# Performance work log

Measured on AMD Instinct MI355X. Metric: run time of the kernel, lower is better.

The kernel has to match this reference:

```python
import jax, jax.numpy as jnp
import numpy as np

FORGET_BIAS = 1.0  # tf.nn.rnn_cell.LSTMCell default

def lstm_scan(x_seq, W, b, reverse=False):
    # x_seq: [B, T, D]; W: [D+U, 4U] with TF gate order (i, j, f, o); b: [4U]
    B = x_seq.shape[0]
    U = b.shape[0] // 4
    xs = jnp.swapaxes(x_seq, 0, 1)  # [T, B, D]

    def step(carry, x_t):
        c, h = carry
        z = jnp.dot(jnp.concatenate([x_t, h], axis=-1), W) + b  # [B, 4U]
        i, j, f, o = jnp.split(z, 4, axis=-1)
        c_new = jax.nn.sigmoid(f + FORGET_BIAS) * c + jax.nn.sigmoid(i) * jnp.tanh(j)
        h_new = jax.nn.sigmoid(o) * jnp.tanh(c_new)
        return (c_new, h_new), h_new

    init = (jnp.zeros((B, U), x_seq.dtype), jnp.zeros((B, U), x_seq.dtype))
    _, hs = jax.lax.scan(step, init, xs, reverse=reverse)  # outputs aligned to time index
    return jnp.swapaxes(hs, 0, 1)  # [B, T, U]

def setup_inputs() -> dict:
    key = jax.random.key(0)
    k1, k2, k3 = jax.random.split(key, 3)
    B, H, W_, C = 64, 8, 512, 64
    D, U = H * C, 256
    scale = 1.0 / np.sqrt(D + U)
    x = jax.random.normal(k1, (B, H, W_, C), dtype=jnp.float32)
    W_fw = jax.random.normal(k2, (D + U, 4 * U), dtype=jnp.float32) * scale
    W_bw = jax.random.normal(k3, (D + U, 4 * U), dtype=jnp.float32) * scale
    b_fw = jnp.zeros((4 * U,), dtype=jnp.float32)
    b_bw = jnp.zeros((4 * U,), dtype=jnp.float32)
    return {"x": x, "W_fw": W_fw, "b_fw": b_fw, "W_bw": W_bw, "b_bw": b_bw}

def reference(x, W_fw, b_fw, W_bw, b_bw):
    b, h, w, c = x.shape
    # dropout is identity at inference (training=False)
    feats = jnp.transpose(x, (0, 2, 1, 3)).reshape(b, w, h * c)  # [B, T, D]
    out_fw = lstm_scan(feats, W_fw, b_fw, reverse=False)
    out_bw = lstm_scan(feats, W_bw, b_bw, reverse=True)
    return jnp.concatenate([out_fw, out_bw], axis=2)  # [B, T, 2U]
```

## Files before the change

### kernel.cpp

```cpp
#include <hip/hip_runtime.h>


typedef float f32x4 __attribute__((ext_vector_type(4)));
typedef _Float16 f16;
typedef _Float16 f16x4 __attribute__((ext_vector_type(4)));
typedef _Float16 f16x8 __attribute__((ext_vector_type(8)));
typedef unsigned int u32;
typedef unsigned int u32x4 __attribute__((ext_vector_type(4)));
typedef unsigned long long u64;

__global__ void init_all(const float* __restrict__ Wfw, const float* __restrict__ Wbw,
                         f16* __restrict__ wrec2, u32* __restrict__ hbuf) {
    const int i = blockIdx.x * blockDim.x + threadIdx.x;
    const int dir = i >> 18;
    const int rem = i & 0x3FFFF;
    const int col = rem >> 8;
    const int k   = rem & 255;
    const int sl  = col >> 7;
    const int gg  = (col & 127) >> 5;
    const int uu  = col & 31;
    const float* W = dir ? Wbw : Wfw;
    wrec2[i] = (f16)W[(size_t)(512 + k) * 1024 + gg * 256 + sl * 32 + uu];
    if (i < 65544) hbuf[i] = 0u;
}

#define BM 128
#define BN 128
#define BK 32
#define ASTR 40

__global__ __launch_bounds__(256)
void gemm_xz(const float* __restrict__ x,
             const float* __restrict__ Wfw, const float* __restrict__ Wbw,
             const float* __restrict__ bfw, const float* __restrict__ bbw,
             f16* __restrict__ xz_fw, f16* __restrict__ xz_bw) {
    const int dir = blockIdx.z;
    const float* __restrict__ W    = dir ? Wbw : Wfw;
    const float* __restrict__ bias = dir ? bbw : bfw;
    f16* __restrict__ xz = dir ? xz_bw : xz_fw;

    __shared__ __align__(16) f16 As[BM * ASTR];
    __shared__ __align__(16) f16 Bs[BN * ASTR];

    const int tid = threadIdx.x;
    const int m0 = blockIdx.x * BM;
    const int n0 = blockIdx.y * BN;

    const int lane = tid & 63;
    const int wave = tid >> 6;
    const int wm = (wave & 1) * 64;
    const int wn = (wave >> 1) * 64;
    const int mi = lane & 15;
    const int kq = lane >> 4;

    const int arow = tid >> 1;
    const int ahalf = (tid & 1) * 16;
    const int am = m0 + arow;
    const int bb = am >> 9;
    const int t  = am & 511;
    const int kk = tid >> 3;
    const int nc = (tid & 7) * 16;

    f32x4 acc[4][4];
#pragma unroll
    for (int i = 0; i < 4; i++)
#pragma unroll
        for (int j = 0; j < 4; j++) acc[i][j] = (f32x4)0.f;

    for (int kt = 0; kt < 512; kt += BK) {
        float va[16], vb[16];
        {
            const int kbase = kt + ahalf;
            const int hh = kbase >> 6;
            const float* px = x + (((size_t)bb * 8 + hh) * 512 + t) * 64 + (kbase & 63);
#pragma unroll
            for (int i = 0; i < 4; i++) {
                f32x4 v = *(const f32x4*)(px + i * 4);
                va[i*4+0] = v[0]; va[i*4+1] = v[1]; va[i*4+2] = v[2]; va[i*4+3] = v[3];
            }
            const float* pw = W + (size_t)(kt + kk) * 1024 + n0 + nc;
#pragma unroll
            for (int i = 0; i < 4; i++) {
                f32x4 v = *(const f32x4*)(pw + i * 4);
                vb[i*4+0] = v[0]; vb[i*4+1] = v[1]; vb[i*4+2] = v[2]; vb[i*4+3] = v[3];
            }
        }
        __syncthreads();
        {
            f16* pa = &As[arow * ASTR + ahalf];
#pragma unroll
            for (int i = 0; i < 4; i++) {
                f16x4 s;
                s[0] = (f16)va[i*4+0]; s[1] = (f16)va[i*4+1];
                s[2] = (f16)va[i*4+2]; s[3] = (f16)va[i*4+3];
                *(f16x4*)(pa + i * 4) = s;
            }
#pragma unroll
            for (int i = 0; i < 16; i++)
                Bs[(nc + i) * ASTR + kk] = (f16)vb[i];
        }
        __syncthreads();
        f16x8 afr[4], bfr[4];
#pragma unroll
        for (int mt = 0; mt < 4; mt++)
            afr[mt] = *(const f16x8*)(&As[(wm + mt * 16 + mi) * ASTR + kq * 8]);
#pragma unroll
        for (int nt = 0; nt < 4; nt++)
            bfr[nt] = *(const f16x8*)(&Bs[(wn + nt * 16 + mi) * ASTR + kq * 8]);
#pragma unroll
        for (int mt = 0; mt < 4; mt++)
#pragma unroll
            for (int nt = 0; nt < 4; nt++)
                acc[mt][nt] = __builtin_amdgcn_mfma_f32_16x16x32_f16(
                    afr[mt], bfr[nt], acc[mt][nt], 0, 0, 0);
    }

    const int col = lane & 15;
    const int rbase = kq * 4;
#pragma unroll
    for (int mt = 0; mt < 4; mt++) {
#pragma unroll
        for (int nt = 0; nt < 4; nt++) {
            const int n = n0 + wn + nt * 16 + col;
            const float bv = bias[n];
#pragma unroll
            for (int r = 0; r < 4; r++) {
                const int mrow = m0 + wm + mt * 16 + rbase + r;
                xz[(size_t)mrow * 1024 + n] = (f16)(acc[mt][nt][r] + bv);
            }
        }
    }
}

#define AP 264
#define ZP 67
#define MAXSPIN 4096

#define POLL16(qv, ap)                                                        \
    asm volatile(                                                             \
        "global_load_dwordx4 %0, %16, off sc0\n\t"                            \
        "global_load_dwordx4 %1, %16, off offset:64 sc0\n\t"                  \
        "global_load_dwordx4 %2, %16, off offset:128 sc0\n\t"                 \
        "global_load_dwordx4 %3, %16, off offset:192 sc0\n\t"                 \
        "global_load_dwordx4 %4, %16, off offset:256 sc0\n\t"                 \
        "global_load_dwordx4 %5, %16, off offset:320 sc0\n\t"                 \
        "global_load_dwordx4 %6, %16, off offset:384 sc0\n\t"                 \
        "global_load_dwordx4 %7, %16, off offset:448 sc0\n\t"                 \
        "global_load_dwordx4 %8, %16, off offset:512 sc0\n\t"                 \
        "global_load_dwordx4 %9, %16, off offset:576 sc0\n\t"                 \
        "global_load_dwordx4 %10, %16, off offset:640 sc0\n\t"                \
        "global_load_dwordx4 %11, %16, off offset:704 sc0\n\t"                \
        "global_load_dwordx4 %12, %16, off offset:768 sc0\n\t"                \
        "global_load_dwordx4 %13, %16, off offset:832 sc0\n\t"                \
        "global_load_dwordx4 %14, %16, off offset:896 sc0\n\t"                \
        "global_load_dwordx4 %15, %16, off offset:960 sc0\n\t"                \
        "s_waitcnt vmcnt(0)"                                                  \
        : "=v"(qv[0]), "=v"(qv[1]), "=v"(qv[2]), "=v"(qv[3]),                 \
          "=v"(qv[4]), "=v"(qv[5]), "=v"(qv[6]), "=v"(qv[7]),                 \
          "=v"(qv[8]), "=v"(qv[9]), "=v"(qv[10]), "=v"(qv[11]),               \
          "=v"(qv[12]), "=v"(qv[13]), "=v"(qv[14]), "=v"(qv[15])              \
        : "v"(ap)                                                             \
        : "memory")

__global__ __launch_bounds__(256, 1)
void rec_persist(const f16* __restrict__ xz, const f16* __restrict__ wrec2,
                 u32* __restrict__ hbuf, u32* __restrict__ claimctr,
                 float* __restrict__ out) {
    __shared__ int cs[2];
    if (threadIdx.x == 0) {
        u32 xcd;
        asm("s_getreg_b32 %0, hwreg(HW_REG_XCC_ID, 0, 32)" : "=s"(xcd));
        int d = -1, slv = 0;
        if (xcd < 2u) {
            u32 slot = atomicAdd(&claimctr[xcd], 1u);
            if (slot < 8u) { d = (int)xcd; slv = (int)slot; }
        }
        cs[0] = d; cs[1] = slv;
    }
    __syncthreads();
    const int dir = cs[0];
    const int sl  = cs[1];
    if (dir < 0) return;

    const f16* __restrict__ xzd = xz + (size_t)dir * 64 * 512 * 1024;
    const f16* __restrict__ wsl = wrec2 + ((size_t)dir * 1024 + sl * 128) * 256;
    u32* __restrict__ hbd = hbuf + (size_t)dir * 2 * 64 * 256;

    __shared__ __align__(16) f16  A_lds[64 * AP];
    __shared__ float z_lds[128 * ZP];

    const int tid = threadIdx.x;
    const int lane = tid & 63;
    const int w = tid >> 6;
    const int r = w >> 1, c = w & 1;
    const int mi = lane & 15, kq = lane >> 4;

    f16x8 Bf[4][8];
#pragma unroll
    for (int nt = 0; nt < 4; nt++)
#pragma unroll
        for (int ks = 0; ks < 8; ks++)
            Bf[nt][ks] = *(const f16x8*)(wsl + (size_t)(c * 64 + nt * 16 + mi) * 256
                                             + ks * 32 + kq * 8);

    const int b_act = tid >> 2;
    const int ug = tid & 3;
    float cell[8];
#pragma unroll
    for (int j = 0; j < 8; j++) cell[j] = 0.f;

    const int sm = tid >> 2;

    float pv[8];
    int   pt = 0;

    float* const outb = out + ((size_t)b_act * 512) * 512 + dir * 256 + sl * 32 + ug * 8;

    for (int s = 0; s < 512; s++) {
        const int t = dir ? (511 - s) : s;

        if (s) {
            float* op = outb + (size_t)pt * 512;
            f32x4 o0 = {pv[0], pv[1], pv[2], pv[3]};
            f32x4 o1 = {pv[4], pv[5], pv[6], pv[7]};
            *(f32x4*)op = o0;
            *(f32x4*)(op + 4) = o1;
        }

        const char* srcb = (const char*)(hbd + (s & 1) * (64 * 256))
                         + (size_t)sm * 1024 + ug * 16;
        const u32 tp = (u32)s << 16;
        u32x4 q[16];
        POLL16(q, srcb);
        int spins = 0;
        for (;;) {
            u32 bad = 0;
#pragma unroll
            for (int i = 0; i < 16; i++) {
                bad |= (q[i][0] ^ tp) & 0xFFFF0000u;
                bad |= (q[i][1] ^ tp) & 0xFFFF0000u;
                bad |= (q[i][2] ^ tp) & 0xFFFF0000u;
                bad |= (q[i][3] ^ tp) & 0xFFFF0000u;
            }
            if (!__any((int)(bad != 0))) break;
            if (++spins > MAXSPIN) break;
            if (spins > 16) __builtin_amdgcn_s_sleep(2);
            POLL16(q, srcb);
        }

        f16x8 xzv[4];
        const f16* xp = xzd + ((size_t)b_act * 512 + t) * 1024 + sl * 32 + ug * 8;
#pragma unroll
        for (int g = 0; g < 4; g++) xzv[g] = *(const f16x8*)(xp + g * 256);

        {
            f16* dst = A_lds + sm * AP;
#pragma unroll
            for (int i = 0; i < 16; i++) {
                u32 p0 = (q[i][0] & 0xFFFFu) | (q[i][1] << 16);
                u32 p1 = (q[i][2] & 0xFFFFu) | (q[i][3] << 16);
                *(u64*)(dst + i * 16 + ug * 4) = (u64)p0 | ((u64)p1 << 32);
            }
        }
        __syncthreads();

        f32x4 acc[2][4];
#pragma unroll
        for (int mt = 0; mt < 2; mt++)
#pragma unroll
            for (int nt = 0; nt < 4; nt++) acc[mt][nt] = (f32x4)0.f;
#pragma unroll
        for (int ks = 0; ks < 8; ks++) {
            f16x8 Af[2];
#pragma unroll
            for (int mt = 0; mt < 2; mt++)
                Af[mt] = *(const f16x8*)(A_lds + (r * 32 + mt * 16 + mi) * AP
                                               + ks * 32 + kq * 8);
#pragma unroll
            for (int mt = 0; mt < 2; mt++)
#pragma unroll
                for (int nt = 0; nt < 4; nt++)
                    acc[mt][nt] = __builtin_amdgcn_mfma_f32_16x16x32_f16(
                        Af[mt], Bf[nt][ks], acc[mt][nt], 0, 0, 0);
        }
#pragma unroll
        for (int mt = 0; mt < 2; mt++)
#pragma unroll
            for (int nt = 0; nt < 4; nt++) {
                const int col = c * 64 + nt * 16 + mi;
                float* zp = z_lds + col * ZP + r * 32 + mt * 16 + kq * 4;
#pragma unroll
                for (int ri = 0; ri < 4; ri++) zp[ri] = acc[mt][nt][ri];
            }
        __syncthreads();

        float hv[8];
#pragma unroll
        for (int j = 0; j < 8; j++) {
            const int uu = ug * 8 + j;
            const float zi = z_lds[(0 * 32 + uu) * ZP + b_act] + (float)xzv[0][j];
            const float zj = z_lds[(1 * 32 + uu) * ZP + b_act] + (float)xzv[1][j];
            const float zf = z_lds[(2 * 32 + uu) * ZP + b_act] + (float)xzv[2][j] + 1.0f;
            const float zo = z_lds[(3 * 32 + uu) * ZP + b_act] + (float)xzv[3][j];
            const float si = 1.f / (1.f + __expf(-zi));
            const float sf = 1.f / (1.f + __expf(-zf));
            const float so = 1.f / (1.f + __expf(-zo));
            const float tj = 1.f - 2.f / (1.f + __expf(2.f * zj));
            cell[j] = sf * cell[j] + si * tj;
            hv[j] = so * (1.f - 2.f / (1.f + __expf(2.f * cell[j])));
        }

        {
            const u32 tg = ((u32)(s + 1)) << 16;
            u32* hwp = hbd + ((s + 1) & 1) * (64 * 256) + b_act * 256 + sl * 32 + ug * 8;
            union { f16 h; unsigned short us; } cv;
            u32x4 st0, st1;
#pragma unroll
            for (int j = 0; j < 4; j++) { cv.h = (f16)hv[j];     st0[j] = (u32)cv.us | tg; }
#pragma unroll
            for (int j = 0; j < 4; j++) { cv.h = (f16)hv[4 + j]; st1[j] = (u32)cv.us | tg; }
            asm volatile(
                "global_store_dwordx4 %0, %1, off sc0\n\t"
                "global_store_dwordx4 %0, %2, off offset:16 sc0"
                :: "v"(hwp), "v"(st0), "v"(st1)
                : "memory");
        }
#pragma unroll
        for (int j = 0; j < 8; j++) pv[j] = hv[j];
        pt = t;
    }
    {
        float* op = outb + (size_t)pt * 512;
        f32x4 o0 = {pv[0], pv[1], pv[2], pv[3]};
        f32x4 o1 = {pv[4], pv[5], pv[6], pv[7]};
        *(f32x4*)op = o0;
        *(f32x4*)(op + 4) = o1;
    }
}

extern "C" void kernel_launch(void* const* d_in, const int* in_sizes, int n_in,
                              void* d_out, int out_size, void* d_ws, size_t ws_size,
                              hipStream_t stream) {
    const float* x   = (const float*)d_in[0];
    const float* Wfw = (const float*)d_in[1];
    const float* bfw = (const float*)d_in[2];
    const float* Wbw = (const float*)d_in[3];
    const float* bbw = (const float*)d_in[4];
    float* out = (float*)d_out;

    f16* xzf   = (f16*)d_ws;
    f16* xzb   = xzf + (size_t)64 * 512 * 1024;
    f16* wrec2 = xzb + (size_t)64 * 512 * 1024;
    u32* hbuf  = (u32*)(wrec2 + (size_t)2 * 1024 * 256);
    u32* claim = hbuf + (size_t)2 * 2 * 64 * 256;

    init_all<<<dim3(2048), 256, 0, stream>>>(Wfw, Wbw, wrec2, hbuf);
    gemm_xz<<<dim3(256, 8, 2), 256, 0, stream>>>(x, Wfw, Wbw, bfw, bbw, xzf, xzb);
    rec_persist<<<dim3(256), 256, 0, stream>>>(xzf, wrec2, hbuf, claim, out);

    (void)in_sizes; (void)n_in; (void)out_size; (void)ws_size;
}
```

Measured before the change: 2.657 ms.

## Batch output stores every 8 steps, poll without sleep, claim one block per CU

The recurrent loop is unrolled in phases of 8 steps. Hidden outputs are buffered in registers and written to global memory once per phase instead of every step. The spin-wait drops its s_sleep backoff and issues the xz loads before the poll loop so their latency overlaps. Block claiming now uses a per-CU occupancy flag (HW_ID) so at most one recurrent block runs per CU, with the zeroed flag region enlarged to match. These trade extra registers and a busier poll for lower per-step latency.

```diff
diff --git a/kernel.cpp b/kernel.cpp
--- a/kernel.cpp
+++ b/kernel.cpp
@@ -21,7 +21,7 @@
     const int uu  = col & 31;
     const float* W = dir ? Wbw : Wfw;
     wrec2[i] = (f16)W[(size_t)(512 + k) * 1024 + gg * 256 + sl * 32 + uu];
-    if (i < 65544) hbuf[i] = 0u;
+    if (i < 66056) hbuf[i] = 0u;
 }
 
 #define BM 128
@@ -134,9 +134,9 @@
 
 #define AP 264
 #define ZP 67
-#define MAXSPIN 4096
-
-#define POLL16(qv, ap)                                                        \
+#define MAXSPIN 4000
+
+#define BULK16(qv, ap)                                                        \
     asm volatile(                                                             \
         "global_load_dwordx4 %0, %16, off sc0\n\t"                            \
         "global_load_dwordx4 %1, %16, off offset:64 sc0\n\t"                  \
@@ -155,10 +155,10 @@
         "global_load_dwordx4 %14, %16, off offset:896 sc0\n\t"                \
         "global_load_dwordx4 %15, %16, off offset:960 sc0\n\t"                \
         "s_waitcnt vmcnt(0)"                                                  \
-        : "=v"(qv[0]), "=v"(qv[1]), "=v"(qv[2]), "=v"(qv[3]),                 \
-          "=v"(qv[4]), "=v"(qv[5]), "=v"(qv[6]), "=v"(qv[7]),                 \
-          "=v"(qv[8]), "=v"(qv[9]), "=v"(qv[10]), "=v"(qv[11]),               \
-          "=v"(qv[12]), "=v"(qv[13]), "=v"(qv[14]), "=v"(qv[15])              \
+        : "=&v"(qv[0]), "=&v"(qv[1]), "=&v"(qv[2]), "=&v"(qv[3]),             \
+          "=&v"(qv[4]), "=&v"(qv[5]), "=&v"(qv[6]), "=&v"(qv[7]),             \
+          "=&v"(qv[8]), "=&v"(qv[9]), "=&v"(qv[10]), "=&v"(qv[11]),           \
+          "=&v"(qv[12]), "=&v"(qv[13]), "=&v"(qv[14]), "=&v"(qv[15])          \
         : "v"(ap)                                                             \
         : "memory")
 
@@ -168,12 +168,16 @@
                  float* __restrict__ out) {
     __shared__ int cs[2];
     if (threadIdx.x == 0) {
-        u32 xcd;
+        u32 xcd, hwid;
         asm("s_getreg_b32 %0, hwreg(HW_REG_XCC_ID, 0, 32)" : "=s"(xcd));
+        asm("s_getreg_b32 %0, hwreg(HW_REG_HW_ID, 8, 8)" : "=s"(hwid));
         int d = -1, slv = 0;
         if (xcd < 2u) {
-            u32 slot = atomicAdd(&claimctr[xcd], 1u);
-            if (slot < 8u) { d = (int)xcd; slv = (int)slot; }
+            u32 occ = atomicExch(&claimctr[8 + xcd * 256 + (hwid & 255u)], 1u);
+            if (occ == 0u) {
+                u32 slot = atomicAdd(&claimctr[xcd], 1u);
+                if (slot < 8u) { d = (int)xcd; slv = (int)slot; }
+            }
         }
         cs[0] = d; cs[1] = slv;
     }
@@ -211,130 +215,138 @@
 
     const int sm = tid >> 2;
 
-    float pv[8];
-    int   pt = 0;
-
+    float pv[8][8];
     float* const outb = out + ((size_t)b_act * 512) * 512 + dir * 256 + sl * 32 + ug * 8;
 
-    for (int s = 0; s < 512; s++) {
-        const int t = dir ? (511 - s) : s;
-
-        if (s) {
-            float* op = outb + (size_t)pt * 512;
-            f32x4 o0 = {pv[0], pv[1], pv[2], pv[3]};
-            f32x4 o1 = {pv[4], pv[5], pv[6], pv[7]};
+    for (int s0 = 0; s0 < 512; s0 += 8) {
+        if (s0) {
+            const int sb = s0 - 8;
+#pragma unroll
+            for (int i = 0; i < 8; i++) {
+                const int tf = dir ? (511 - (sb + i)) : (sb + i);
+                float* op = outb + (size_t)tf * 512;
+                f32x4 o0 = {pv[i][0], pv[i][1], pv[i][2], pv[i][3]};
+                f32x4 o1 = {pv[i][4], pv[i][5], pv[i][6], pv[i][7]};
+                *(f32x4*)op = o0;
+                *(f32x4*)(op + 4) = o1;
+            }
+        }
+
+#pragma unroll
+        for (int ph = 0; ph < 8; ph++) {
+            const int s = s0 + ph;
+            const int t = dir ? (511 - s) : s;
+            const u32 tp = (u32)s << 16;
+
+            const char* srcb = (const char*)(hbd + (ph & 1) * (64 * 256))
+                             + (size_t)sm * 1024 + ug * 16;
+            u32x4 q[16];
+            BULK16(q, srcb);
+
+            f16x8 xzv[4];
+            const f16* xp = xzd + ((size_t)b_act * 512 + t) * 1024 + sl * 32 + ug * 8;
+#pragma unroll
+            for (int g = 0; g < 4; g++) xzv[g] = *(const f16x8*)(xp + g * 256);
+
+            int spins = 0;
+            for (;;) {
+                u32 bad = 0;
+#pragma unroll
+                for (int i = 0; i < 16; i++)
+                    bad |= (q[i][0] ^ tp) | (q[i][1] ^ tp)
+                         | (q[i][2] ^ tp) | (q[i][3] ^ tp);
+                if (!__any((int)((bad & 0xFFFF0000u) != 0))) break;
+                if (++spins > MAXSPIN) break;
+                BULK16(q, srcb);
+            }
+
+            {
+                f16* dst = A_lds + sm * AP;
+#pragma unroll
+                for (int i = 0; i < 16; i++) {
+                    u32 p0 = (q[i][0] & 0xFFFFu) | (q[i][1] << 16);
+                    u32 p1 = (q[i][2] & 0xFFFFu) | (q[i][3] << 16);
+                    *(u64*)(dst + i * 16 + ug * 4) = (u64)p0 | ((u64)p1 << 32);
+                }
+            }
+            __syncthreads();
+
+            f32x4 acc[2][4];
+#pragma unroll
+            for (int mt = 0; mt < 2; mt++)
+#pragma unroll
+                for (int nt = 0; nt < 4; nt++) acc[mt][nt] = (f32x4)0.f;
+#pragma unroll
+            for (int ks = 0; ks < 8; ks++) {
+                f16x8 Af[2];
+#pragma unroll
+                for (int mt = 0; mt < 2; mt++)
+                    Af[mt] = *(const f16x8*)(A_lds + (r * 32 + mt * 16 + mi) * AP
+                                                   + ks * 32 + kq * 8);
+#pragma unroll
+                for (int mt = 0; mt < 2; mt++)
+#pragma unroll
+                    for (int nt = 0; nt < 4; nt++)
+                        acc[mt][nt] = __builtin_amdgcn_mfma_f32_16x16x32_f16(
+                            Af[mt], Bf[nt][ks], acc[mt][nt], 0, 0, 0);
+            }
+#pragma unroll
+            for (int mt = 0; mt < 2; mt++)
+#pragma unroll
+                for (int nt = 0; nt < 4; nt++) {
+                    const int col = c * 64 + nt * 16 + mi;
+                    float* zp = z_lds + col * ZP + r * 32 + mt * 16 + kq * 4;
+#pragma unroll
+                    for (int ri = 0; ri < 4; ri++) zp[ri] = acc[mt][nt][ri];
+                }
+            __syncthreads();
+
+            float hv[8];
+#pragma unroll
+            for (int j = 0; j < 8; j++) {
+                const int uu = ug * 8 + j;
+                const float zi = z_lds[(0 * 32 + uu) * ZP + b_act] + (float)xzv[0][j];
+                const float zj = z_lds[(1 * 32 + uu) * ZP + b_act] + (float)xzv[1][j];
+                const float zf = z_lds[(2 * 32 + uu) * ZP + b_act] + (float)xzv[2][j] + 1.0f;
+                const float zo = z_lds[(3 * 32 + uu) * ZP + b_act] + (float)xzv[3][j];
+                const float si = 1.f / (1.f + __expf(-zi));
+                const float sf = 1.f / (1.f + __expf(-zf));
+                const float so = 1.f / (1.f + __expf(-zo));
+                const float tj = 1.f - 2.f / (1.f + __expf(2.f * zj));
+                cell[j] = sf * cell[j] + si * tj;
+                hv[j] = so * (1.f - 2.f / (1.f + __expf(2.f * cell[j])));
+            }
+
+            {
+                const u32 tg = ((u32)(s + 1)) << 16;
+                union { f16 h; unsigned short us; } cv;
+                u32x4 st0, st1;
+#pragma unroll
+                for (int j = 0; j < 4; j++) { cv.h = (f16)hv[j];     st0[j] = (u32)cv.us | tg; }
+#pragma unroll
+                for (int j = 0; j < 4; j++) { cv.h = (f16)hv[4 + j]; st1[j] = (u32)cv.us | tg; }
+                u32* hwp = hbd + ((ph + 1) & 1) * (64 * 256) + b_act * 256 + sl * 32 + ug * 8;
+                asm volatile(
+                    "global_store_dwordx4 %0, %1, off sc0\n\t"
+                    "global_store_dwordx4 %0, %2, off offset:16 sc0"
+                    :: "v"(hwp), "v"(st0), "v"(st1)
+                    : "memory");
+            }
+#pragma unroll
+            for (int j = 0; j < 8; j++) pv[ph][j] = hv[j];
+        }
+    }
+    {
+        const int sb = 504;
+#pragma unroll
+        for (int i = 0; i < 8; i++) {
+            const int tf = dir ? (511 - (sb + i)) : (sb + i);
+            float* op = outb + (size_t)tf * 512;
+            f32x4 o0 = {pv[i][0], pv[i][1], pv[i][2], pv[i][3]};
+            f32x4 o1 = {pv[i][4], pv[i][5], pv[i][6], pv[i][7]};
             *(f32x4*)op = o0;
             *(f32x4*)(op + 4) = o1;
         }
-
-        const char* srcb = (const char*)(hbd + (s & 1) * (64 * 256))
-                         + (size_t)sm * 1024 + ug * 16;
-        const u32 tp = (u32)s << 16;
-        u32x4 q[16];
-        POLL16(q, srcb);
-        int spins = 0;
-        for (;;) {
-            u32 bad = 0;
-#pragma unroll
-            for (int i = 0; i < 16; i++) {
-                bad |= (q[i][0] ^ tp) & 0xFFFF0000u;
-                bad |= (q[i][1] ^ tp) & 0xFFFF0000u;
-                bad |= (q[i][2] ^ tp) & 0xFFFF0000u;
-                bad |= (q[i][3] ^ tp) & 0xFFFF0000u;
-            }
-            if (!__any((int)(bad != 0))) break;
-            if (++spins > MAXSPIN) break;
-            if (spins > 16) __builtin_amdgcn_s_sleep(2);
-            POLL16(q, srcb);
-        }
-
-        f16x8 xzv[4];
-        const f16* xp = xzd + ((size_t)b_act * 512 + t) * 1024 + sl * 32 + ug * 8;
-#pragma unroll
-        for (int g = 0; g < 4; g++) xzv[g] = *(const f16x8*)(xp + g * 256);
-
-        {
-            f16* dst = A_lds + sm * AP;
-#pragma unroll
-            for (int i = 0; i < 16; i++) {
-                u32 p0 = (q[i][0] & 0xFFFFu) | (q[i][1] << 16);
-                u32 p1 = (q[i][2] & 0xFFFFu) | (q[i][3] << 16);
-                *(u64*)(dst + i * 16 + ug * 4) = (u64)p0 | ((u64)p1 << 32);
-            }
-        }
-        __syncthreads();
-
-        f32x4 acc[2][4];
-#pragma unroll
-        for (int mt = 0; mt < 2; mt++)
-#pragma unroll
-            for (int nt = 0; nt < 4; nt++) acc[mt][nt] = (f32x4)0.f;
-#pragma unroll
-        for (int ks = 0; ks < 8; ks++) {
-            f16x8 Af[2];
-#pragma unroll
-            for (int mt = 0; mt < 2; mt++)
-                Af[mt] = *(const f16x8*)(A_lds + (r * 32 + mt * 16 + mi) * AP
-                                               + ks * 32 + kq * 8);
-#pragma unroll
-            for (int mt = 0; mt < 2; mt++)
-#pragma unroll
-                for (int nt = 0; nt < 4; nt++)
-                    acc[mt][nt] = __builtin_amdgcn_mfma_f32_16x16x32_f16(
-                        Af[mt], Bf[nt][ks], acc[mt][nt], 0, 0, 0);
-        }
-#pragma unroll
-        for (int mt = 0; mt < 2; mt++)
-#pragma unroll
-            for (int nt = 0; nt < 4; nt++) {
-                const int col = c * 64 + nt * 16 + mi;
-                float* zp = z_lds + col * ZP + r * 32 + mt * 16 + kq * 4;
-#pragma unroll
-                for (int ri = 0; ri < 4; ri++) zp[ri] = acc[mt][nt][ri];
-            }
-        __syncthreads();
-
-        float hv[8];
-#pragma unroll
-        for (int j = 0; j < 8; j++) {
-            const int uu = ug * 8 + j;
-            const float zi = z_lds[(0 * 32 + uu) * ZP + b_act] + (float)xzv[0][j];
-            const float zj = z_lds[(1 * 32 + uu) * ZP + b_act] + (float)xzv[1][j];
-            const float zf = z_lds[(2 * 32 + uu) * ZP + b_act] + (float)xzv[2][j] + 1.0f;
-            const float zo = z_lds[(3 * 32 + uu) * ZP + b_act] + (float)xzv[3][j];
-            const float si = 1.f / (1.f + __expf(-zi));
-            const float sf = 1.f / (1.f + __expf(-zf));
-            const float so = 1.f / (1.f + __expf(-zo));
-            const float tj = 1.f - 2.f / (1.f + __expf(2.f * zj));
-            cell[j] = sf * cell[j] + si * tj;
-            hv[j] = so * (1.f - 2.f / (1.f + __expf(2.f * cell[j])));
-        }
-
-        {
-            const u32 tg = ((u32)(s + 1)) << 16;
-            u32* hwp = hbd + ((s + 1) & 1) * (64 * 256) + b_act * 256 + sl * 32 + ug * 8;
-            union { f16 h; unsigned short us; } cv;
-            u32x4 st0, st1;
-#pragma unroll
-            for (int j = 0; j < 4; j++) { cv.h = (f16)hv[j];     st0[j] = (u32)cv.us | tg; }
-#pragma unroll
-            for (int j = 0; j < 4; j++) { cv.h = (f16)hv[4 + j]; st1[j] = (u32)cv.us | tg; }
-            asm volatile(
-                "global_store_dwordx4 %0, %1, off sc0\n\t"
-                "global_store_dwordx4 %0, %2, off offset:16 sc0"
-                :: "v"(hwp), "v"(st0), "v"(st1)
-                : "memory");
-        }
-#pragma unroll
-        for (int j = 0; j < 8; j++) pv[j] = hv[j];
-        pt = t;
-    }
-    {
-        float* op = outb + (size_t)pt * 512;
-        f32x4 o0 = {pv[0], pv[1], pv[2], pv[3]};
-        f32x4 o1 = {pv[4], pv[5], pv[6], pv[7]};
-        *(f32x4*)op = o0;
-        *(f32x4*)(op + 4) = o1;
     }
 }
 
```

After: 2.660 ms. Within noise of the previous version (+0.1%).
